# Optimization experiments

Hardware: AMD Instinct MI355X
Metric: run time of the kernel (lower is better)

The kernel has to match this reference:

```python
import jax, jax.numpy as jnp
import numpy as np

B, D_IN, D_OUT = 8192, 4096, 4096
IN_DIMS = (64, 64)
OUT_DIMS = (64, 64)
# tt_rank_rate=0.5 over dims [64,64,64,64] -> ranks [1,32,1024,32,1]
RANKS = (1, 32, 1024, 32, 1)


def _kaiming_uniform(key, shape):
    # matches nn.init.kaiming_uniform_(a=sqrt(5)) on a (r_prev, d, r) tensor:
    # fan_in = prod(shape[1:]) = d * r, gain = sqrt(2/(1+5)) = sqrt(1/3)
    fan_in = shape[1] * shape[2]
    bound = np.sqrt(1.0 / 3.0) * np.sqrt(3.0 / fan_in)
    return jax.random.uniform(key, shape, jnp.float32, -bound, bound)


def setup_inputs() -> dict:
    key = jax.random.key(0)
    kx, k0, k1, k2, k3, kb = jax.random.split(key, 6)
    dims = list(IN_DIMS) + list(OUT_DIMS)
    shapes = [(RANKS[i], dims[i], RANKS[i + 1]) for i in range(4)]
    x = jax.random.normal(kx, (B, D_IN), jnp.float32)
    core0 = _kaiming_uniform(k0, shapes[0])  # (1, 64, 32)
    core1 = _kaiming_uniform(k1, shapes[1])  # (32, 64, 1024)
    core2 = _kaiming_uniform(k2, shapes[2])  # (1024, 64, 32)
    core3 = _kaiming_uniform(k3, shapes[3])  # (32, 64, 1)
    bb = 1.0 / np.sqrt(D_IN)
    bias = jax.random.uniform(kb, (D_OUT,), jnp.float32, -bb, bb)
    return {"x": x, "core0": core0, "core1": core1, "core2": core2,
            "core3": core3, "bias": bias}


def reference(x, core0, core1, core2, core3, bias):
    b = x.shape[0]
    s = x.reshape(b, IN_DIMS[0], IN_DIMS[1])          # (B, 64, 64)
    # input core 0: contract first input dim (rank-in = 1 squeezed)
    s = jnp.einsum('bcd,cs->bds', s, core0[0])        # (B, 64, 32)
    # input core 1: contract second input dim and rank
    s = jnp.einsum('bcr,rcs->bs', s, core1)           # (B, 1024)
    # output core 2: expand first output dim
    s = jnp.einsum('br,rAs->bAs', s, core2)           # (B, 64, 32)
    # output core 3: expand second output dim (rank-out = 1 squeezed)
    s = jnp.einsum('bAr,rB->bAB', s, core3[..., 0])   # (B, 64, 64)
    return s.reshape(b, -1) + bias                    # (B, 4096)
```

## Files before the change

### kernel.cpp

```cpp
#include <hip/hip_runtime.h>
#include <hip/hip_bf16.h>


typedef _Float16 h4 __attribute__((ext_vector_type(4)));
typedef _Float16 h8 __attribute__((ext_vector_type(8)));
typedef float f32x4 __attribute__((ext_vector_type(4)));

#define BATCH 8192

__device__ __forceinline__ void gld_lds16(const void* g, void* l) {
  __builtin_amdgcn_global_load_lds(
      (__attribute__((address_space(1))) void*)(g),
      (__attribute__((address_space(3))) void*)(l), 16, 0, 0);
}

__global__ __launch_bounds__(256) void transpose_cast2(
    const float* __restrict__ c1, _Float16* __restrict__ W1t,
    const float* __restrict__ c2, _Float16* __restrict__ W2t) {
  __shared__ float t[64][65];
  const int which = blockIdx.z;
  const float* src = which ? c2 : c1;
  _Float16* dst = which ? W2t : W1t;
  const int K = which ? 1024 : 2048, U = which ? 2048 : 1024;
  const int k0 = (which ? blockIdx.y : blockIdx.x) * 64;
  const int u0 = (which ? blockIdx.x : blockIdx.y) * 64;
  const int tx = threadIdx.x & 63, ty = threadIdx.x >> 6;
  for (int i = ty; i < 64; i += 4) {
    const int k = k0 + i;
    const int sr = which ? k : ((k & 31) * 64 + (k >> 5));
    t[i][tx] = src[(size_t)sr * U + u0 + tx];
  }
  __syncthreads();
  for (int i = ty; i < 64; i += 4) {
    dst[(size_t)(u0 + i) * K + k0 + tx] = (_Float16)t[tx][i];
  }
}

__global__ __launch_bounds__(256) void stage2(const float* __restrict__ x,
                                              const float* __restrict__ c0,
                                              _Float16* __restrict__ s1) {
  __shared__ _Float16 xh[4 * 4096];
  __shared__ float c0l[2048];
  const int b0 = blockIdx.x * 4;
  const int tid = threadIdx.x;

  {
    const float4* xg = (const float4*)(x + (size_t)b0 * 4096);
#pragma unroll
    for (int k = 0; k < 16; ++k) {
      float4 v = xg[tid + 256 * k];
      h4 w = {(_Float16)v.x, (_Float16)v.y, (_Float16)v.z, (_Float16)v.w};
      ((h4*)xh)[tid + 256 * k] = w;
    }
    ((float4*)c0l)[tid] = ((const float4*)c0)[tid];
    ((float4*)c0l)[tid + 256] = ((const float4*)c0)[tid + 256];
  }
  __syncthreads();

  const int row = tid >> 6, t6 = tid & 63;
  const int d0 = (t6 >> 3) * 8;
  const int r0 = (t6 & 7) * 4;
  const _Float16* xrow = xh + row * 4096;

  float acc[8][4];
#pragma unroll
  for (int i = 0; i < 8; ++i)
#pragma unroll
    for (int j = 0; j < 4; ++j) acc[i][j] = 0.0f;

  for (int c = 0; c < 64; ++c) {
    h8 xv = *(const h8*)&xrow[c * 64 + d0];
    f32x4 wv = *(const f32x4*)&c0l[c * 32 + r0];
#pragma unroll
    for (int i = 0; i < 8; ++i) {
      const float xf = (float)xv[i];
#pragma unroll
      for (int j = 0; j < 4; ++j) acc[i][j] += xf * wv[j];
    }
  }

  _Float16* s1row = s1 + (size_t)(b0 + row) * 2048;
#pragma unroll
  for (int i = 0; i < 8; ++i) {
    h4 o = {(_Float16)acc[i][0], (_Float16)acc[i][1], (_Float16)acc[i][2],
            (_Float16)acc[i][3]};
    *(h4*)&s1row[(d0 + i) * 32 + r0] = o;
  }
}

template <int K, int CN>
__global__ __launch_bounds__(512, 2) void gemm_pipe(
    const _Float16* __restrict__ A, const _Float16* __restrict__ Bt,
    _Float16* __restrict__ C) {
  __shared__ __align__(16) char lds[3 * 49152];
  constexpr int NT = K / 64;
  const int bm = blockIdx.x, bn = blockIdx.y;
  const int tid = threadIdx.x;
  const int w = tid >> 6, lane = tid & 63;
  const int lr = lane & 15, kh = lane >> 4;
  const int wmo = (w >> 2) << 6, wno = (w & 3) << 6;

  f32x4 acc[4][4] = {};

  const int sr = tid >> 3;
  const int sc = ((tid & 7) ^ (sr & 7)) << 4;
  const char* gA = (const char*)(A + (size_t)(bm * 128 + sr) * K) + sc;
  const char* gB = (const char*)(Bt + (size_t)(bn * 256 + sr) * K) + sc;
  const size_t rk = (size_t)K * 128;
  char* lw = lds + (w << 10);

  auto STAGE_A = [&](int t) {
    char* b_ = lw + (t % 3) * 49152;
    const char* ga = gA + (size_t)t * 128;
    gld_lds16(ga, b_);
    gld_lds16(ga + rk, b_ + 8192);
    gld_lds16(gB + (size_t)t * 128, b_ + 16384);
  };
  auto STAGE_B = [&](int t) {
    char* b_ = lw + (t % 3) * 49152;
    const char* gb = gB + (size_t)t * 128;
    gld_lds16(gb + rk, b_ + 24576);
    gld_lds16(gb + 2 * rk, b_ + 32768);
    gld_lds16(gb + 3 * rk, b_ + 40960);
  };

  auto KTILE = [&](int t, bool last) {
    if (last)
      asm volatile("s_waitcnt vmcnt(0)" ::: "memory");
    else
      asm volatile("s_waitcnt vmcnt(6)" ::: "memory");
    __builtin_amdgcn_s_barrier();
    __builtin_amdgcn_sched_barrier(0);
    const char* bufA = lds + (t % 3) * 49152;
    const char* bufB = bufA + 16384;
    h8 af[2][4], bf[2][4];
#pragma unroll
    for (int kk = 0; kk < 2; ++kk) {
#pragma unroll
      for (int m = 0; m < 4; ++m) {
        const int R = wmo + m * 16 + lr;
        af[kk][m] = *(const h8*)(bufA + R * 128 +
                                 ((((kk << 2) + kh) ^ (R & 7)) << 4));
      }
#pragma unroll
      for (int n = 0; n < 2; ++n) {
        const int R = wno + n * 16 + lr;
        bf[kk][n] = *(const h8*)(bufB + R * 128 +
                                 ((((kk << 2) + kh) ^ (R & 7)) << 4));
      }
    }
    if (t + 2 < NT) STAGE_A(t + 2);
    asm volatile("s_waitcnt lgkmcnt(0)" ::: "memory");
    __builtin_amdgcn_sched_barrier(0);
    __builtin_amdgcn_s_setprio(1);
#pragma unroll
    for (int kk = 0; kk < 2; ++kk)
#pragma unroll
      for (int m = 0; m < 4; ++m)
#pragma unroll
        for (int n = 0; n < 2; ++n)
          acc[m][n] = __builtin_amdgcn_mfma_f32_16x16x32_f16(
              af[kk][m], bf[kk][n], acc[m][n], 0, 0, 0);
    __builtin_amdgcn_s_setprio(0);
    __builtin_amdgcn_s_barrier();
    __builtin_amdgcn_sched_barrier(0);
#pragma unroll
    for (int kk = 0; kk < 2; ++kk)
#pragma unroll
      for (int n = 2; n < 4; ++n) {
        const int R = wno + n * 16 + lr;
        bf[kk][n] = *(const h8*)(bufB + R * 128 +
                                 ((((kk << 2) + kh) ^ (R & 7)) << 4));
      }
    if (t + 2 < NT) STAGE_B(t + 2);
    asm volatile("s_waitcnt lgkmcnt(0)" ::: "memory");
    __builtin_amdgcn_sched_barrier(0);
    __builtin_amdgcn_s_setprio(1);
#pragma unroll
    for (int kk = 0; kk < 2; ++kk)
#pragma unroll
      for (int m = 0; m < 4; ++m)
#pragma unroll
        for (int n = 2; n < 4; ++n)
          acc[m][n] = __builtin_amdgcn_mfma_f32_16x16x32_f16(
              af[kk][m], bf[kk][n], acc[m][n], 0, 0, 0);
    __builtin_amdgcn_s_setprio(0);
  };

  STAGE_A(0); STAGE_B(0);
  STAGE_A(1); STAGE_B(1);
  for (int t = 0; t < NT - 1; ++t) KTILE(t, false);
  KTILE(NT - 1, true);

#pragma unroll
  for (int m = 0; m < 4; ++m) {
    const int r0 = bm * 128 + wmo + m * 16 + kh * 4;
#pragma unroll
    for (int n = 0; n < 4; ++n) {
      const int c0 = bn * 256 + wno + n * 16 + lr;
#pragma unroll
      for (int q = 0; q < 4; ++q)
        C[(size_t)(r0 + q) * CN + c0] = (_Float16)acc[m][n][q];
    }
  }
}

template <int K>
__global__ __launch_bounds__(512, 2) void gemm2_8ph(
    const _Float16* __restrict__ A, const _Float16* __restrict__ Bt,
    const float* __restrict__ c3, const float* __restrict__ bias,
    float* __restrict__ out) {
  __shared__ __align__(16) char lds[131072];
  constexpr int NT = K / 64;
  const int bm = blockIdx.x, bn = blockIdx.y;
  const int tid = threadIdx.x;
  const int w = tid >> 6, lane = tid & 63;
  const int lr = lane & 15, kh = lane >> 4;
  const int l7 = lr & 7;

  f32x4 acc[8][4] = {};

  const int sr = tid >> 3;
  const int sc = ((tid & 7) ^ (sr & 7)) << 4;
  const size_t rowK = (size_t)K * 2;
  const char* gA = (const char*)A + (size_t)(bm * 256 + sr) * rowK + sc;
  const char* gB = (const char*)Bt + (size_t)(bn * 256 + sr) * rowK + sc;
  char* lw = lds + (w << 10);

  auto STAGE = [&](int kind, int t) {
    char* d = lw + kind * 32768 + (t & 1) * 16384;
    const char* g = (kind < 2 ? gA : gB) + (size_t)(kind & 1) * 128 * rowK +
                    (size_t)t * 128;
    gld_lds16(g, d);
    gld_lds16(g + 64 * rowK, d + 8192);
  };

  const char* bufA0 = lds + (w >> 2) * 32768;
  const char* bufB0 = lds + 65536 + ((w & 3) >> 1) * 32768;
  const int bcol = (w & 1) * 64;

  h8 af[2][4], bflo[2][2], bfhi[2][2];

  STAGE(0, 0); STAGE(1, 0); STAGE(2, 0); STAGE(3, 0);
  STAGE(2, 1); STAGE(0, 1); STAGE(1, 1);
  asm volatile("s_waitcnt vmcnt(6)" ::: "memory");
  __builtin_amdgcn_sched_barrier(0);
  __builtin_amdgcn_s_barrier();

  for (int t = 0; t < NT; ++t) {
    const char* bA = bufA0 + (t & 1) * 16384;
    const char* bB = bufB0 + (t & 1) * 16384;
#pragma unroll
    for (int kk = 0; kk < 2; ++kk) {
#pragma unroll
      for (int m = 0; m < 4; ++m)
        af[kk][m] = *(const h8*)(bA + (m * 16 + lr) * 128 +
                                 ((((kk << 2) + kh) ^ l7) << 4));
#pragma unroll
      for (int n = 0; n < 2; ++n)
        bflo[kk][n] = *(const h8*)(bB + (bcol + n * 16 + lr) * 128 +
                                   ((((kk << 2) + kh) ^ l7) << 4));
    }
    if (t + 1 < NT) STAGE(3, t + 1);
    __builtin_amdgcn_sched_barrier(0);
    __builtin_amdgcn_s_barrier();
    asm volatile("s_waitcnt lgkmcnt(0)" ::: "memory");
    __builtin_amdgcn_sched_barrier(0);
    __builtin_amdgcn_s_setprio(1);
#pragma unroll
    for (int kk = 0; kk < 2; ++kk)
#pragma unroll
      for (int m = 0; m < 4; ++m)
#pragma unroll
        for (int n = 0; n < 2; ++n)
          acc[m][n] = __builtin_amdgcn_mfma_f32_16x16x32_f16(
              af[kk][m], bflo[kk][n], acc[m][n], 0, 0, 0);
    __builtin_amdgcn_s_setprio(0);
    __builtin_amdgcn_s_barrier();
#pragma unroll
    for (int kk = 0; kk < 2; ++kk)
#pragma unroll
      for (int n = 0; n < 2; ++n)
        bfhi[kk][n] = *(const h8*)(bB + (bcol + 32 + n * 16 + lr) * 128 +
                                   ((((kk << 2) + kh) ^ l7) << 4));
    if (t + 2 < NT) STAGE(2, t + 2);
    __builtin_amdgcn_sched_barrier(0);
    __builtin_amdgcn_s_barrier();
    asm volatile("s_waitcnt lgkmcnt(0)" ::: "memory");
    __builtin_amdgcn_sched_barrier(0);
    __builtin_amdgcn_s_setprio(1);
#pragma unroll
    for (int kk = 0; kk < 2; ++kk)
#pragma unroll
      for (int m = 0; m < 4; ++m)
#pragma unroll
        for (int n = 0; n < 2; ++n)
          acc[m][2 + n] = __builtin_amdgcn_mfma_f32_16x16x32_f16(
              af[kk][m], bfhi[kk][n], acc[m][2 + n], 0, 0, 0);
    __builtin_amdgcn_s_setprio(0);
    __builtin_amdgcn_s_barrier();
#pragma unroll
    for (int kk = 0; kk < 2; ++kk)
#pragma unroll
      for (int m = 0; m < 4; ++m)
        af[kk][m] = *(const h8*)(bA + (64 + m * 16 + lr) * 128 +
                                 ((((kk << 2) + kh) ^ l7) << 4));
    __builtin_amdgcn_sched_barrier(0);
    __builtin_amdgcn_s_barrier();
    asm volatile("s_waitcnt lgkmcnt(0)" ::: "memory");
    __builtin_amdgcn_sched_barrier(0);
    __builtin_amdgcn_s_setprio(1);
#pragma unroll
    for (int kk = 0; kk < 2; ++kk)
#pragma unroll
      for (int m = 0; m < 4; ++m)
#pragma unroll
        for (int n = 0; n < 2; ++n)
          acc[4 + m][n] = __builtin_amdgcn_mfma_f32_16x16x32_f16(
              af[kk][m], bflo[kk][n], acc[4 + m][n], 0, 0, 0);
    __builtin_amdgcn_s_setprio(0);
    __builtin_amdgcn_s_barrier();
    if (t + 2 < NT) { STAGE(0, t + 2); STAGE(1, t + 2); }
    __builtin_amdgcn_sched_barrier(0);
    __builtin_amdgcn_s_barrier();
    __builtin_amdgcn_s_setprio(1);
#pragma unroll
    for (int kk = 0; kk < 2; ++kk)
#pragma unroll
      for (int m = 0; m < 4; ++m)
#pragma unroll
        for (int n = 0; n < 2; ++n)
          acc[4 + m][2 + n] = __builtin_amdgcn_mfma_f32_16x16x32_f16(
              af[kk][m], bfhi[kk][n], acc[4 + m][2 + n], 0, 0, 0);
    __builtin_amdgcn_s_setprio(0);
    if (t + 2 < NT)
      asm volatile("s_waitcnt vmcnt(6)" ::: "memory");
    else
      asm volatile("s_waitcnt vmcnt(0)" ::: "memory");
    __builtin_amdgcn_sched_barrier(0);
    __builtin_amdgcn_s_barrier();
  }

  h8 bfe[4];
  float bb[8][4];
#pragma unroll
  for (int n = 0; n < 4; ++n) {
#pragma unroll
    for (int j = 0; j < 8; ++j)
      bfe[n][j] = (_Float16)c3[(kh * 8 + j) * 64 + n * 16 + lr];
#pragma unroll
    for (int a = 0; a < 8; ++a)
      bb[a][n] = bias[(bn * 8 + a) * 64 + n * 16 + lr];
  }
  __syncthreads();
  {
    const int wmo = (w >> 2) << 7;
    const int wno = (w & 3) << 6;
#pragma unroll
    for (int m = 0; m < 8; ++m) {
      const int Rb = wmo + m * 16 + kh * 4;
#pragma unroll
      for (int n = 0; n < 4; ++n) {
        const int cc = wno + n * 16 + lr;
#pragma unroll
        for (int q = 0; q < 4; ++q) {
          const int R = Rb + q;
          *(_Float16*)(lds + R * 512 +
                       ((((cc >> 3) ^ (R & 7)) << 4) | ((cc & 7) << 1))) =
              (_Float16)acc[m][n][q];
        }
      }
    }
  }
  __syncthreads();
  const int r32 = w << 5;
#pragma unroll
  for (int mi = 0; mi < 2; ++mi) {
    const int rr = r32 + mi * 16 + lr;
    const int orow0 = bm * 256 + r32 + mi * 16 + (kh << 2);
#pragma unroll
    for (int a = 0; a < 8; ++a) {
      h8 afv = *(const h8*)(lds + rr * 512 +
                            ((((a * 4 + kh) ^ (rr & 7)) << 4)));
#pragma unroll
      for (int n = 0; n < 4; ++n) {
        f32x4 d = {};
        d = __builtin_amdgcn_mfma_f32_16x16x32_f16(afv, bfe[n], d, 0, 0, 0);
        const int ocol = (bn * 8 + a) * 64 + n * 16 + lr;
#pragma unroll
        for (int q = 0; q < 4; ++q)
          out[(size_t)(orow0 + q) * 4096 + ocol] = d[q] + bb[a][n];
      }
    }
  }
}

extern "C" void kernel_launch(void* const* d_in, const int* in_sizes, int n_in,
                              void* d_out, int out_size, void* d_ws,
                              size_t ws_size, hipStream_t stream) {
  (void)in_sizes; (void)n_in; (void)out_size; (void)ws_size;
  const float* x     = (const float*)d_in[0];
  const float* core0 = (const float*)d_in[1];
  const float* core1 = (const float*)d_in[2];
  const float* core2 = (const float*)d_in[3];
  const float* core3 = (const float*)d_in[4];
  const float* bias  = (const float*)d_in[5];
  float* out = (float*)d_out;

  char* ws = (char*)d_ws;
  _Float16* s1h = (_Float16*)ws;
  _Float16* s2h = (_Float16*)(ws + 33554432);
  _Float16* W1t = (_Float16*)(ws + 50331648);
  _Float16* W2t = (_Float16*)(ws + 54525952);

  transpose_cast2<<<dim3(32, 16, 2), 256, 0, stream>>>(core1, W1t, core2, W2t);
  stage2<<<BATCH / 4, 256, 0, stream>>>(x, core0, s1h);
  gemm_pipe<2048, 1024><<<dim3(BATCH / 128, 4), 512, 0, stream>>>(s1h, W1t, s2h);
  gemm2_8ph<1024><<<dim3(BATCH / 256, 2048 / 256), 512, 0, stream>>>(
      s2h, W2t, core3, bias, out);
}
```

Measured before the change: 149.1 us.

## Widen stage2 blocks, swizzle GEMM block order, vectorize final epilogue stores

Stage2 now runs 512 threads per block, each computing a 4x4 tile, to raise parallelism. Both GEMMs map a 1D grid through an XCD-aware swizzle so that co-resident blocks share A/B tiles in L2. The final epilogue swaps the MFMA operands so each lane holds four contiguous output columns. It seeds the accumulator with a vector bias load and writes float4 stores instead of scattered scalar stores. The swizzle is hardcoded to a 256-block grid.

```diff
diff --git a/kernel.cpp b/kernel.cpp
--- a/kernel.cpp
+++ b/kernel.cpp
@@ -2,6 +2,7 @@
 #include <hip/hip_bf16.h>
 
 
+typedef _Float16 h2 __attribute__((ext_vector_type(2)));
 typedef _Float16 h4 __attribute__((ext_vector_type(4)));
 typedef _Float16 h8 __attribute__((ext_vector_type(8)));
 typedef float f32x4 __attribute__((ext_vector_type(4)));
@@ -36,7 +37,7 @@
   }
 }
 
-__global__ __launch_bounds__(256) void stage2(const float* __restrict__ x,
+__global__ __launch_bounds__(512) void stage2(const float* __restrict__ x,
                                               const float* __restrict__ c0,
                                               _Float16* __restrict__ s1) {
   __shared__ _Float16 xh[4 * 4096];
@@ -47,32 +48,26 @@
   {
     const float4* xg = (const float4*)(x + (size_t)b0 * 4096);
 #pragma unroll
-    for (int k = 0; k < 16; ++k) {
-      float4 v = xg[tid + 256 * k];
+    for (int k = 0; k < 8; ++k) {
+      float4 v = xg[tid + 512 * k];
       h4 w = {(_Float16)v.x, (_Float16)v.y, (_Float16)v.z, (_Float16)v.w};
-      ((h4*)xh)[tid + 256 * k] = w;
+      ((h4*)xh)[tid + 512 * k] = w;
     }
     ((float4*)c0l)[tid] = ((const float4*)c0)[tid];
-    ((float4*)c0l)[tid + 256] = ((const float4*)c0)[tid + 256];
   }
   __syncthreads();
 
-  const int row = tid >> 6, t6 = tid & 63;
-  const int d0 = (t6 >> 3) * 8;
-  const int r0 = (t6 & 7) * 4;
+  const int row = tid >> 7, t7 = tid & 127;
+  const int d0 = (t7 >> 3) * 4;
+  const int r0 = (t7 & 7) * 4;
   const _Float16* xrow = xh + row * 4096;
 
-  float acc[8][4];
-#pragma unroll
-  for (int i = 0; i < 8; ++i)
-#pragma unroll
-    for (int j = 0; j < 4; ++j) acc[i][j] = 0.0f;
-
+  float acc[4][4] = {};
   for (int c = 0; c < 64; ++c) {
-    h8 xv = *(const h8*)&xrow[c * 64 + d0];
+    h4 xv = *(const h4*)&xrow[c * 64 + d0];
     f32x4 wv = *(const f32x4*)&c0l[c * 32 + r0];
 #pragma unroll
-    for (int i = 0; i < 8; ++i) {
+    for (int i = 0; i < 4; ++i) {
       const float xf = (float)xv[i];
 #pragma unroll
       for (int j = 0; j < 4; ++j) acc[i][j] += xf * wv[j];
@@ -81,20 +76,22 @@
 
   _Float16* s1row = s1 + (size_t)(b0 + row) * 2048;
 #pragma unroll
-  for (int i = 0; i < 8; ++i) {
+  for (int i = 0; i < 4; ++i) {
     h4 o = {(_Float16)acc[i][0], (_Float16)acc[i][1], (_Float16)acc[i][2],
             (_Float16)acc[i][3]};
     *(h4*)&s1row[(d0 + i) * 32 + r0] = o;
   }
 }
 
-template <int K, int CN>
+template <int K, int CN, int NBM>
 __global__ __launch_bounds__(512, 2) void gemm_pipe(
     const _Float16* __restrict__ A, const _Float16* __restrict__ Bt,
     _Float16* __restrict__ C) {
   __shared__ __align__(16) char lds[3 * 49152];
   constexpr int NT = K / 64;
-  const int bm = blockIdx.x, bn = blockIdx.y;
+  const int lin = blockIdx.x;
+  const int swz = (lin & 7) * 32 + (lin >> 3);
+  const int bm = swz % NBM, bn = swz / NBM;
   const int tid = threadIdx.x;
   const int w = tid >> 6, lane = tid & 63;
   const int lr = lane & 15, kh = lane >> 4;
@@ -205,14 +202,16 @@
   }
 }
 
-template <int K>
+template <int K, int NBM>
 __global__ __launch_bounds__(512, 2) void gemm2_8ph(
     const _Float16* __restrict__ A, const _Float16* __restrict__ Bt,
     const float* __restrict__ c3, const float* __restrict__ bias,
     float* __restrict__ out) {
   __shared__ __align__(16) char lds[131072];
   constexpr int NT = K / 64;
-  const int bm = blockIdx.x, bn = blockIdx.y;
+  const int lin = blockIdx.x;
+  const int swz = (lin & 7) * 32 + (lin >> 3);
+  const int bm = swz % NBM, bn = swz / NBM;
   const int tid = threadIdx.x;
   const int w = tid >> 6, lane = tid & 63;
   const int lr = lane & 15, kh = lane >> 4;
@@ -342,16 +341,11 @@
   }
 
   h8 bfe[4];
-  float bb[8][4];
-#pragma unroll
-  for (int n = 0; n < 4; ++n) {
+#pragma unroll
+  for (int n = 0; n < 4; ++n)
 #pragma unroll
     for (int j = 0; j < 8; ++j)
       bfe[n][j] = (_Float16)c3[(kh * 8 + j) * 64 + n * 16 + lr];
-#pragma unroll
-    for (int a = 0; a < 8; ++a)
-      bb[a][n] = bias[(bn * 8 + a) * 64 + n * 16 + lr];
-  }
   __syncthreads();
   {
     const int wmo = (w >> 2) << 7;
@@ -375,21 +369,22 @@
   __syncthreads();
   const int r32 = w << 5;
 #pragma unroll
-  for (int mi = 0; mi < 2; ++mi) {
-    const int rr = r32 + mi * 16 + lr;
-    const int orow0 = bm * 256 + r32 + mi * 16 + (kh << 2);
-#pragma unroll
-    for (int a = 0; a < 8; ++a) {
+  for (int a = 0; a < 8; ++a) {
+    f32x4 bs[4];
+#pragma unroll
+    for (int n = 0; n < 4; ++n)
+      bs[n] = *(const f32x4*)&bias[(bn * 8 + a) * 64 + n * 16 + kh * 4];
+#pragma unroll
+    for (int mi = 0; mi < 2; ++mi) {
+      const int rr = r32 + mi * 16 + lr;
       h8 afv = *(const h8*)(lds + rr * 512 +
                             ((((a * 4 + kh) ^ (rr & 7)) << 4)));
+      const size_t orow = (size_t)(bm * 256 + r32 + mi * 16 + lr);
 #pragma unroll
       for (int n = 0; n < 4; ++n) {
-        f32x4 d = {};
-        d = __builtin_amdgcn_mfma_f32_16x16x32_f16(afv, bfe[n], d, 0, 0, 0);
-        const int ocol = (bn * 8 + a) * 64 + n * 16 + lr;
-#pragma unroll
-        for (int q = 0; q < 4; ++q)
-          out[(size_t)(orow0 + q) * 4096 + ocol] = d[q] + bb[a][n];
+        f32x4 d = __builtin_amdgcn_mfma_f32_16x16x32_f16(bfe[n], afv, bs[n],
+                                                         0, 0, 0);
+        *(f32x4*)&out[orow * 4096 + (bn * 8 + a) * 64 + n * 16 + kh * 4] = d;
       }
     }
   }
@@ -414,8 +409,7 @@
   _Float16* W2t = (_Float16*)(ws + 54525952);
 
   transpose_cast2<<<dim3(32, 16, 2), 256, 0, stream>>>(core1, W1t, core2, W2t);
-  stage2<<<BATCH / 4, 256, 0, stream>>>(x, core0, s1h);
-  gemm_pipe<2048, 1024><<<dim3(BATCH / 128, 4), 512, 0, stream>>>(s1h, W1t, s2h);
-  gemm2_8ph<1024><<<dim3(BATCH / 256, 2048 / 256), 512, 0, stream>>>(
-      s2h, W2t, core3, bias, out);
-}
+  stage2<<<BATCH / 4, 512, 0, stream>>>(x, core0, s1h);
+  gemm_pipe<2048, 1024, 64><<<256, 512, 0, stream>>>(s1h, W1t, s2h);
+  gemm2_8ph<1024, 32><<<256, 512, 0, stream>>>(s2h, W2t, core3, bias, out);
+}
```

New measurement: 158.8 us. 6.5% more time.
